# Kernel optimization log

Measured on AMD Instinct MI355X. Metric: run time of the kernel, lower is better.

## Reference

```python
import jax, jax.numpy as jnp
import numpy as np

B, S, H = 2, 1024, 2048
HEADS = 16
QC = 1536      # q_compressed_dim
KVC = 512      # kv_compressed_dim
ROPE = 64      # qk_rope_dim
NOPE = H // HEADS  # 128, non-rope head dim
VH = 128       # v_head_dim
INTER = 1408   # MoE intermediate dim
NSH = 2        # shared experts
NRT = 8        # routed experts
TOPK = 2
EPS = 1e-6


def setup_inputs() -> dict:
    key = jax.random.key(0)
    ks = jax.random.split(key, 16)

    def w(k, shape, scale=0.02):
        return jax.random.normal(k, shape, jnp.float32) * scale

    return {
        "x": jax.random.normal(ks[0], (B, S, H), jnp.float32),
        "freq": jax.random.uniform(ks[1], (S, ROPE // 2), jnp.float32, 0.0, 2.0 * np.pi),
        "mask": jnp.zeros((S, S), jnp.float32),
        "w_attn_norm": jnp.ones((H,), jnp.float32),
        "w_ffn_norm": jnp.ones((H,), jnp.float32),
        "W_dq": w(ks[2], (H, QC)),
        "q_c_norm": jnp.ones((QC,), jnp.float32),
        "W_uq": w(ks[3], (QC, HEADS * (NOPE + ROPE))),
        "W_dkv": w(ks[4], (H, KVC + ROPE)),
        "kv_c_norm": jnp.ones((KVC,), jnp.float32),
        "W_ukv": w(ks[5], (KVC, HEADS * (NOPE + VH))),
        "W_o": w(ks[6], (HEADS * VH, H)),
        "W_r": w(ks[7], (H, NRT)),
        "Ws_gate": w(ks[8], (NSH, H, INTER)),
        "Ws_up": w(ks[9], (NSH, H, INTER)),
        "Ws_down": w(ks[10], (NSH, INTER, H)),
        "We_gate": w(ks[11], (NRT, H, INTER)),
        "We_up": w(ks[12], (NRT, H, INTER)),
        "We_down": w(ks[13], (NRT, INTER, H)),
    }


def rmsnorm(x, w):
    return x * jax.lax.rsqrt(jnp.mean(x * x, axis=-1, keepdims=True) + EPS) * w


def rope_apply(x, cos, sin):
    # x: [..., S, D]; cos/sin: [S, D/2], interleaved-pair rotation
    x1 = x[..., 0::2]
    x2 = x[..., 1::2]
    return jnp.stack([x1 * cos - x2 * sin, x1 * sin + x2 * cos], axis=-1).reshape(x.shape)


def _experts(t, Wg, Wu, Wd):
    # t: [T,H]; W*: [E,H,I]/[E,I,H] -> [E,T,H], SwiGLU per expert
    hid = jax.nn.silu(jnp.einsum('th,ehi->eti', t, Wg)) * jnp.einsum('th,ehi->eti', t, Wu)
    return jnp.einsum('eti,eih->eth', hid, Wd)


def reference(x, freq, mask, w_attn_norm, w_ffn_norm, W_dq, q_c_norm, W_uq, W_dkv,
              kv_c_norm, W_ukv, W_o, W_r, Ws_gate, Ws_up, Ws_down,
              We_gate, We_up, We_down):
    Bb, Ss, Hh = x.shape
    cos = jnp.cos(freq)
    sin = jnp.sin(freq)

    # ---- MLA attention (pre-norm) ----
    h = rmsnorm(x, w_attn_norm)
    cq = rmsnorm(h @ W_dq, q_c_norm)                              # [B,S,QC]
    q = (cq @ W_uq).reshape(Bb, Ss, HEADS, NOPE + ROPE).transpose(0, 2, 1, 3)
    q_nope, q_rope = q[..., :NOPE], q[..., NOPE:]
    q_rope = rope_apply(q_rope, cos, sin)                          # [B,Hh,S,ROPE]

    ckv = h @ W_dkv                                               # [B,S,KVC+ROPE]
    kv_c = rmsnorm(ckv[..., :KVC], kv_c_norm)
    k_rope = rope_apply(ckv[..., KVC:], cos, sin)                  # [B,S,ROPE] shared over heads
    kv = (kv_c @ W_ukv).reshape(Bb, Ss, HEADS, NOPE + VH).transpose(0, 2, 1, 3)
    k_nope, v = kv[..., :NOPE], kv[..., NOPE:]

    scale = 1.0 / np.sqrt(NOPE + ROPE)
    scores = (jnp.einsum('bhsd,bhtd->bhst', q_nope, k_nope)
              + jnp.einsum('bhsd,btd->bhst', q_rope, k_rope)) * scale + mask
    attn = jax.nn.softmax(scores, axis=-1)
    attn_out = jnp.einsum('bhst,bhtd->bshd', attn, v).reshape(Bb, Ss, HEADS * VH) @ W_o
    x = x + attn_out

    # ---- DeepSeekMoE FFN (pre-norm) ----
    t = rmsnorm(x, w_ffn_norm).reshape(Bb * Ss, Hh)
    shared = _experts(t, Ws_gate, Ws_up, Ws_down).sum(axis=0)      # [T,H]
    probs = jax.nn.softmax(t @ W_r, axis=-1)                       # [T,E]
    vals, idx = jax.lax.top_k(probs, TOPK)
    weights = (jax.nn.one_hot(idx, NRT, dtype=t.dtype) * vals[..., None]).sum(axis=1)  # [T,E]
    routed = jnp.einsum('eth,te->th', _experts(t, We_gate, We_up, We_down), weights)
    return x + (shared + routed).reshape(Bb, Ss, Hh)
```

## Files before the change

### kernel.cpp

```cpp
#include <hip/hip_runtime.h>

typedef __bf16 bf16;
typedef _Float16 f16;
typedef unsigned short u16;
typedef __bf16 bf16x8 __attribute__((ext_vector_type(8)));
typedef _Float16 f16x8 __attribute__((ext_vector_type(8)));
typedef unsigned short u16x8 __attribute__((ext_vector_type(8)));
typedef float f32x4 __attribute__((ext_vector_type(4)));

#define TOK   2048
#define SEQ   1024
#define HIDD  2048
#define NHEADS 16
#define QCD   1536
#define KVCD  512
#define ROPED 64
#define NOPED 128
#define QDIM  192
#define VHD   128
#define KVD   576
#define KVDP  640
#define INTERD 1408
#define GUD   2816
#define RMS_EPS 1e-6f
#define SPS   64.0f
#define OSC   (1.0f/4096.0f)

__device__ inline void split64(float v, f16& h, f16& l) {
    v *= SPS; h = (f16)v; l = (f16)(v - (float)h);
}

__device__ inline void gl_lds16(const void* g, void* l) {
    __builtin_amdgcn_global_load_lds(
        (const __attribute__((address_space(1))) void*)g,
        (__attribute__((address_space(3))) void*)l,
        16, 0, 0);
}

#define WAITN(N) asm volatile("s_waitcnt vmcnt(" #N ")" ::: "memory")

__global__ __launch_bounds__(256) void tconv_ex3_kernel(const float* __restrict__ gate,
                                                        const float* __restrict__ up,
                                                        const float* __restrict__ down,
                                                        bf16* __restrict__ dGU,
                                                        bf16* __restrict__ dD) {
    const float* src; bf16* dst; int K, N;
    if (blockIdx.z == 0)      { src = gate; dst = dGU;                          K = HIDD;   N = INTERD; }
    else if (blockIdx.z == 1) { src = up;   dst = dGU + (size_t)INTERD * HIDD;  K = HIDD;   N = INTERD; }
    else                      { src = down; dst = dD;                           K = INTERD; N = HIDD; }
    int nb = blockIdx.x * 32, kb = blockIdx.y * 32;
    if (nb >= N || kb >= K) return;
    __shared__ float tile[32][33];
    int tx = threadIdx.x & 31, ty = threadIdx.x >> 5;
#pragma unroll
    for (int i = 0; i < 32; i += 8)
        tile[ty + i][tx] = src[(long)(kb + ty + i) * N + nb + tx];
    __syncthreads();
#pragma unroll
    for (int i = 0; i < 32; i += 8)
        dst[(long)(nb + ty + i) * K + kb + tx] = (bf16)tile[tx][ty + i];
}

__global__ __launch_bounds__(256) void tconv3h_kernel(const float* __restrict__ src,
                                                      f16* __restrict__ dst,
                                                      int K, int N, int Npad) {
    __shared__ float tile[32][33];
    int nb = blockIdx.x * 32, kb = blockIdx.y * 32;
    int tx = threadIdx.x & 31, ty = threadIdx.x >> 5;
#pragma unroll
    for (int i = 0; i < 32; i += 8) {
        int k = kb + ty + i, n = nb + tx;
        tile[ty + i][tx] = (k < K && n < N) ? src[(long)k * N + n] : 0.f;
    }
    __syncthreads();
#pragma unroll
    for (int i = 0; i < 32; i += 8) {
        int n = nb + ty + i, k = kb + tx;
        if (n < Npad && k < K) {
            f16 h, l; split64(tile[tx][ty + i], h, l);
            long base = (long)n * (3 * K) + k;
            dst[base] = h; dst[base + K] = l; dst[base + 2 * K] = h;
        }
    }
}

template<int F16, int TM, int TN>
__global__ __launch_bounds__(256) void gemm_bt_kernel(
    const u16* __restrict__ A, const u16* __restrict__ B, void* __restrict__ Cv,
    const float* __restrict__ aux, const int* __restrict__ idx,
    const int* __restrict__ cntPtr,
    int K, int lda, int ldb, int ldc,
    long sA, long sB, long sC,
    int mode, int auxLd, float osc)
{
    constexpr int AM = TM / 32;
    constexpr int AN = TN / 32;
    constexpr int NBUF = (TM + TN > 192) ? 2 : 3;
    constexpr int PF = NBUF - 1;
    constexpr int L = TM / 32 + TN / 32;
    __shared__ u16 As[NBUF][TM * 64];
    __shared__ u16 Bs[NBUF][TN * 64];
    const int bn = blockIdx.x, bm = blockIdx.y, z = blockIdx.z;
    int cnt = 1 << 30;
    if (cntPtr) {
        cnt = *cntPtr;
        int pad = (cnt + TM - 1) & ~(TM - 1);
        if (bm * TM >= pad) return;
    }
    const int tid = threadIdx.x, lane = tid & 63, w = tid >> 6;
    const int wm = w >> 1, wn = w & 1;
    const int lr = lane & 15;
    const int srow = lane >> 3, c16 = lane & 7;
    const u16* Ab = A + (long)z * sA + (long)bm * TM * lda;
    const u16* Bb = B + (long)z * sB + (long)bn * TN * ldb;
    f32x4 acc[AM][AN] = {};

    auto stage = [&](int buf, int k0) {
#pragma unroll
        for (int i = 0; i < TM / 32; i++) {
            int rb = i * 32 + w * 8;
            int row = rb + srow;
            int gc = ((c16 ^ (row & 7)) << 3);
            gl_lds16(&Ab[(long)row * lda + k0 + gc], &As[buf][rb * 64]);
        }
#pragma unroll
        for (int i = 0; i < TN / 32; i++) {
            int rb = i * 32 + w * 8;
            int row = rb + srow;
            int gc = ((c16 ^ (row & 7)) << 3);
            gl_lds16(&Bb[(long)row * ldb + k0 + gc], &Bs[buf][rb * 64]);
        }
    };

    const int nk = K >> 6;
#pragma unroll
    for (int p = 0; p < PF; ++p) if (p < nk) stage(p, p << 6);

    for (int t = 0; t < nk; ++t) {
        if (t + PF < nk) stage((t + PF) % NBUF, (t + PF) << 6);
        const int inflight = (nk - 1 - t < PF) ? (nk - 1 - t) : PF;
        if (inflight >= 2) {
            if constexpr (L == 4) WAITN(8); else if constexpr (L == 6) WAITN(12); else WAITN(16);
        } else if (inflight == 1) {
            if constexpr (L == 4) WAITN(4); else if constexpr (L == 6) WAITN(6); else WAITN(8);
        } else {
            WAITN(0);
        }
        __builtin_amdgcn_s_barrier();
        __builtin_amdgcn_sched_barrier(0);
        const int cur = t % NBUF;
#pragma unroll
        for (int ks = 0; ks < 2; ks++) {
            u16x8 af[AM], bfr[AN];
#pragma unroll
            for (int mi = 0; mi < AM; mi++) {
                int row = wm * (TM / 2) + mi * 16 + lr;
                int cg = (ks * 4 + (lane >> 4)) ^ (row & 7);
                af[mi] = *(const u16x8*)&As[cur][row * 64 + cg * 8];
            }
#pragma unroll
            for (int ni = 0; ni < AN; ni++) {
                int row = wn * (TN / 2) + ni * 16 + lr;
                int cg = (ks * 4 + (lane >> 4)) ^ (row & 7);
                bfr[ni] = *(const u16x8*)&Bs[cur][row * 64 + cg * 8];
            }
#pragma unroll
            for (int mi = 0; mi < AM; mi++)
#pragma unroll
                for (int ni = 0; ni < AN; ni++) {
                    if constexpr (F16)
                        acc[mi][ni] = __builtin_amdgcn_mfma_f32_16x16x32_f16(
                            __builtin_bit_cast(f16x8, af[mi]),
                            __builtin_bit_cast(f16x8, bfr[ni]), acc[mi][ni], 0, 0, 0);
                    else
                        acc[mi][ni] = __builtin_amdgcn_mfma_f32_16x16x32_bf16(
                            __builtin_bit_cast(bf16x8, af[mi]),
                            __builtin_bit_cast(bf16x8, bfr[ni]), acc[mi][ni], 0, 0, 0);
                }
        }
        __builtin_amdgcn_s_barrier();
    }

    const int r0 = (lane >> 4) << 2;
    const int rowBase = bm * TM + wm * (TM / 2);
    const int colBase = bn * TN + wn * (TN / 2);
#pragma unroll
    for (int mi = 0; mi < AM; mi++) {
#pragma unroll
        for (int ni = 0; ni < AN; ni++) {
#pragma unroll
            for (int r = 0; r < 4; r++) {
                int row = rowBase + mi * 16 + r0 + r;
                int col = colBase + ni * 16 + lr;
                float val = acc[mi][ni][r] * osc;
                long ci = (long)z * sC + (long)row * ldc + col;
                if (mode == 0) {
                    ((float*)Cv)[ci] = val;
                } else if (mode == 2) {
                    ((float*)Cv)[ci] = val + aux[(long)row * auxLd + col];
                } else if (mode == 3) {
                    float s = aux ? aux[(long)row * auxLd] : 1.f;
                    ((float*)Cv)[ci] += s * val;
                } else if (mode == 5) {
                    if (row < cnt) {
                        int tok = idx[row];
                        ((float*)Cv)[(long)tok * ldc + col] += aux[(long)tok * auxLd] * val;
                    }
                } else {
                    f16 h = (f16)val; f16 l = (f16)(val - (float)h);
                    ((f16*)Cv)[ci] = h; ((f16*)Cv)[ci + auxLd] = h; ((f16*)Cv)[ci + 2 * auxLd] = l;
                }
            }
        }
    }
}

__global__ __launch_bounds__(256) void rmsnorm_kernel(const float* __restrict__ in,
                                                      const float* __restrict__ w,
                                                      bf16* __restrict__ outB,
                                                      float* __restrict__ copyOut, int C) {
    long row = blockIdx.x;
    const float* r = in + row * C;
    float ss = 0.f;
    for (int i = threadIdx.x; i < C; i += 256) { float v = r[i]; ss += v * v; }
    for (int off = 32; off > 0; off >>= 1) ss += __shfl_down(ss, off, 64);
    __shared__ float red[5];
    int lane = threadIdx.x & 63, wv = threadIdx.x >> 6;
    if (lane == 0) red[wv] = ss;
    __syncthreads();
    if (threadIdx.x == 0) red[4] = rsqrtf((red[0] + red[1] + red[2] + red[3]) / C + RMS_EPS);
    __syncthreads();
    float sc = red[4];
    for (int i = threadIdx.x; i < C; i += 256) {
        outB[row * C + i] = (bf16)(r[i] * sc * w[i]);
        if (copyOut) copyOut[row * C + i] = r[i];
    }
}

__global__ __launch_bounds__(256) void rmsnorm3h_kernel(const float* __restrict__ in,
                                                        const float* __restrict__ w,
                                                        f16* __restrict__ out3, int C) {
    long row = blockIdx.x;
    const float* r = in + row * C;
    float ss = 0.f;
    for (int i = threadIdx.x; i < C; i += 256) { float v = r[i]; ss += v * v; }
    for (int off = 32; off > 0; off >>= 1) ss += __shfl_down(ss, off, 64);
    __shared__ float red[5];
    int lane = threadIdx.x & 63, wv = threadIdx.x >> 6;
    if (lane == 0) red[wv] = ss;
    __syncthreads();
    if (threadIdx.x == 0) red[4] = rsqrtf((red[0] + red[1] + red[2] + red[3]) / C + RMS_EPS);
    __syncthreads();
    float sc = red[4];
    f16* o = out3 + row * (3L * C);
    for (int i = threadIdx.x; i < C; i += 256) {
        f16 h, l; split64(r[i] * sc * w[i], h, l);
        o[i] = h; o[C + i] = h; o[2 * C + i] = l;
    }
}

__global__ __launch_bounds__(256) void kvsplit3h_kernel(const float* __restrict__ ckv,
                                                        const float* __restrict__ nrm,
                                                        const float* __restrict__ freq,
                                                        f16* __restrict__ kvc3,
                                                        float* __restrict__ krope) {
    int t = blockIdx.x; int s = t & (SEQ - 1);
    const float* r = ckv + (long)t * KVDP;
    float ss = 0.f;
    for (int i = threadIdx.x; i < KVCD; i += 256) { float v = r[i]; ss += v * v; }
    for (int off = 32; off > 0; off >>= 1) ss += __shfl_down(ss, off, 64);
    __shared__ float red[5];
    int lane = threadIdx.x & 63, wv = threadIdx.x >> 6;
    if (lane == 0) red[wv] = ss;
    __syncthreads();
    if (threadIdx.x == 0) red[4] = rsqrtf((red[0] + red[1] + red[2] + red[3]) / KVCD + RMS_EPS);
    __syncthreads();
    float sc = red[4];
    f16* o = kvc3 + (long)t * (3 * KVCD);
    for (int i = threadIdx.x; i < KVCD; i += 256) {
        f16 h, l; split64(r[i] * sc * nrm[i], h, l);
        o[i] = h; o[KVCD + i] = h; o[2 * KVCD + i] = l;
    }
    if (threadIdx.x < 32) {
        int i = threadIdx.x;
        float f = freq[s * 32 + i], c = cosf(f), sn = sinf(f);
        float x1 = r[KVCD + 2 * i], x2 = r[KVCD + 2 * i + 1];
        krope[(long)t * ROPED + 2 * i]     = x1 * c - x2 * sn;
        krope[(long)t * ROPED + 2 * i + 1] = x1 * sn + x2 * c;
    }
}

__global__ __launch_bounds__(256) void build_q3h_kernel(const float* __restrict__ qpre,
                                                        const float* __restrict__ freq,
                                                        f16* __restrict__ q3) {
    int t = blockIdx.x; int b = t >> 10, s = t & (SEQ - 1);
    for (int idx = threadIdx.x; idx < NHEADS * 96; idx += 256) {
        int h = idx / 96, j = idx % 96;
        const float* qrow = qpre + (long)t * 3072 + h * QDIM;
        f16* dst = q3 + ((long)(b * NHEADS + h) * SEQ + s) * (3 * QDIM);
        if (j < 64) {
            int d = 2 * j;
#pragma unroll
            for (int u = 0; u < 2; u++) {
                f16 hh, ll; split64(qrow[d + u], hh, ll);
                dst[d + u] = hh; dst[QDIM + d + u] = hh; dst[2 * QDIM + d + u] = ll;
            }
        } else {
            int i = j - 64;
            float f = freq[s * 32 + i], c = cosf(f), sn = sinf(f);
            float x1 = qrow[NOPED + 2 * i], x2 = qrow[NOPED + 2 * i + 1];
            float v0 = x1 * c - x2 * sn, v1 = x1 * sn + x2 * c;
            int d = NOPED + 2 * i;
            f16 h0, l0, h1, l1; split64(v0, h0, l0); split64(v1, h1, l1);
            dst[d] = h0; dst[QDIM + d] = h0; dst[2 * QDIM + d] = l0;
            dst[d + 1] = h1; dst[QDIM + d + 1] = h1; dst[2 * QDIM + d + 1] = l1;
        }
    }
}

__global__ __launch_bounds__(256) void build_k3h_kernel(const float* __restrict__ kv,
                                                        const float* __restrict__ krope,
                                                        f16* __restrict__ k3,
                                                        f16* __restrict__ v3T) {
    int t = blockIdx.x; int b = t >> 10, s = t & (SEQ - 1);
    const float* kvrow = kv + (long)t * 4096;
    const float* kr = krope + (long)t * ROPED;
    for (int idx = threadIdx.x; idx < NHEADS * 96; idx += 256) {
        int h = idx / 96, j = idx % 96;
        f16* dst = k3 + ((long)(b * NHEADS + h) * SEQ + s) * (3 * QDIM);
        float v0, v1; int d;
        if (j < 64) { d = 2 * j; v0 = kvrow[h * 256 + d]; v1 = kvrow[h * 256 + d + 1]; }
        else { int i = j - 64; d = NOPED + 2 * i; v0 = kr[2 * i]; v1 = kr[2 * i + 1]; }
        f16 h0, l0, h1, l1; split64(v0, h0, l0); split64(v1, h1, l1);
        dst[d] = h0; dst[QDIM + d] = l0; dst[2 * QDIM + d] = h0;
        dst[d + 1] = h1; dst[QDIM + d + 1] = l1; dst[2 * QDIM + d + 1] = h1;
    }
    for (int idx = threadIdx.x; idx < NHEADS * VHD; idx += 256) {
        int h = idx >> 7, d = idx & 127;
        f16 hh, ll; split64(kvrow[h * 256 + NOPED + d], hh, ll);
        long base = ((long)(b * NHEADS + h) * VHD + d) * (3 * SEQ) + s;
        v3T[base] = hh; v3T[base + SEQ] = ll; v3T[base + 2 * SEQ] = hh;
    }
}

__global__ __launch_bounds__(256) void softmax3h_kernel(const float* __restrict__ scores,
                                                        const float* __restrict__ mask,
                                                        f16* __restrict__ P3, float scale) {
    int s = blockIdx.x, h = blockIdx.y;
    const float* row  = scores + ((long)h * SEQ + s) * SEQ;
    const float* mrow = mask + (long)s * SEQ;
    f16* prow = P3 + ((long)h * SEQ + s) * (3 * SEQ);
    float v[4]; float m = -1e30f;
#pragma unroll
    for (int j = 0; j < 4; j++) {
        int i = threadIdx.x + j * 256;
        v[j] = row[i] * scale + mrow[i];
        m = fmaxf(m, v[j]);
    }
    for (int off = 32; off > 0; off >>= 1) m = fmaxf(m, __shfl_down(m, off, 64));
    __shared__ float redm[5], reds[5];
    int lane = threadIdx.x & 63, wv = threadIdx.x >> 6;
    if (lane == 0) redm[wv] = m;
    __syncthreads();
    if (threadIdx.x == 0) redm[4] = fmaxf(fmaxf(redm[0], redm[1]), fmaxf(redm[2], redm[3]));
    __syncthreads();
    float M = redm[4];
    float sum = 0.f;
#pragma unroll
    for (int j = 0; j < 4; j++) { v[j] = expf(v[j] - M); sum += v[j]; }
    for (int off = 32; off > 0; off >>= 1) sum += __shfl_down(sum, off, 64);
    if (lane == 0) reds[wv] = sum;
    __syncthreads();
    if (threadIdx.x == 0) reds[4] = reds[0] + reds[1] + reds[2] + reds[3];
    __syncthreads();
    float inv = 1.f / reds[4];
#pragma unroll
    for (int j = 0; j < 4; j++) {
        int i = threadIdx.x + j * 256;
        f16 hh, ll; split64(v[j] * inv, hh, ll);
        prow[i] = hh; prow[SEQ + i] = hh; prow[2 * SEQ + i] = ll;
    }
}

__global__ void zero_counts_kernel(int* counts) {
    if (threadIdx.x < 8) counts[threadIdx.x] = 0;
}

__global__ __launch_bounds__(64) void router_kernel(const float* __restrict__ x2,
                                                    const float* __restrict__ wffn,
                                                    const float* __restrict__ Wr,
                                                    float* __restrict__ wts,
                                                    int* __restrict__ perm,
                                                    int* __restrict__ counts) {
    int t = blockIdx.x; int lane = threadIdx.x;
    const float* r = x2 + (long)t * HIDD;
    float ss = 0.f;
    for (int k = lane; k < HIDD; k += 64) { float v = r[k]; ss += v * v; }
    for (int off = 32; off > 0; off >>= 1) ss += __shfl_down(ss, off, 64);
    float sc = rsqrtf(__shfl(ss, 0, 64) / HIDD + RMS_EPS);
    float acc[8] = {0, 0, 0, 0, 0, 0, 0, 0};
    for (int k = lane; k < HIDD; k += 64) {
        float tv = r[k] * sc * wffn[k];
        const float* wr = Wr + (long)k * 8;
#pragma unroll
        for (int e = 0; e < 8; e++) acc[e] += tv * wr[e];
    }
#pragma unroll
    for (int e = 0; e < 8; e++)
        for (int off = 32; off > 0; off >>= 1) acc[e] += __shfl_down(acc[e], off, 64);
    if (lane == 0) {
        float m = acc[0];
#pragma unroll
        for (int e = 1; e < 8; e++) m = fmaxf(m, acc[e]);
        float p[8]; float se = 0.f;
#pragma unroll
        for (int e = 0; e < 8; e++) { p[e] = expf(acc[e] - m); se += p[e]; }
        float inv = 1.f / se;
        int i1 = 0; float v1 = p[0];
        for (int e = 1; e < 8; e++) if (p[e] > v1) { v1 = p[e]; i1 = e; }
        int i2 = -1; float v2 = -1.f;
        for (int e = 0; e < 8; e++) if (e != i1 && p[e] > v2) { v2 = p[e]; i2 = e; }
#pragma unroll
        for (int e = 0; e < 8; e++)
            wts[(long)t * 8 + e] = (e == i1) ? v1 * inv : ((e == i2) ? v2 * inv : 0.f);
        int s1 = atomicAdd(&counts[i1], 1); perm[i1 * TOK + s1] = t;
        int s2 = atomicAdd(&counts[i2], 1); perm[i2 * TOK + s2] = t;
    }
}

__global__ __launch_bounds__(256) void gather_kernel(const bf16* __restrict__ tbuf,
                                                     const int* __restrict__ perm,
                                                     const int* __restrict__ cntPtr,
                                                     bf16* __restrict__ tA) {
    int row = blockIdx.x;
    int cnt = *cntPtr;
    int pad = (cnt + 127) & ~127;
    if (row >= pad) return;
    int i = threadIdx.x * 8;
    if (row < cnt) {
        int tok = perm[row];
        *(bf16x8*)&tA[(long)row * HIDD + i] = *(const bf16x8*)&tbuf[(long)tok * HIDD + i];
    } else {
        bf16x8 z = {};
        *(bf16x8*)&tA[(long)row * HIDD + i] = z;
    }
}

__global__ __launch_bounds__(256) void silumul_kernel(const float* __restrict__ gu,
                                                      bf16* __restrict__ hid,
                                                      const int* __restrict__ cntPtr) {
    long t = blockIdx.x;
    if (cntPtr) {
        int pad = (*cntPtr + 127) & ~127;
        if (t >= pad) return;
    }
    const float* row = gu + t * GUD;
    bf16* h = hid + t * INTERD;
    for (int i = threadIdx.x; i < INTERD; i += 256) {
        float g = row[i], u = row[INTERD + i];
        h[i] = (bf16)(g / (1.f + expf(-g)) * u);
    }
}

static inline size_t alignup(size_t v) { return (v + 255) & ~(size_t)255; }

extern "C" void kernel_launch(void* const* d_in, const int* in_sizes, int n_in,
                              void* d_out, int out_size, void* d_ws, size_t ws_size,
                              hipStream_t stream) {
    const float* x       = (const float*)d_in[0];
    const float* freq    = (const float*)d_in[1];
    const float* mask    = (const float*)d_in[2];
    const float* w_attn  = (const float*)d_in[3];
    const float* w_ffn   = (const float*)d_in[4];
    const float* W_dq    = (const float*)d_in[5];
    const float* q_c_nrm = (const float*)d_in[6];
    const float* W_uq    = (const float*)d_in[7];
    const float* W_dkv   = (const float*)d_in[8];
    const float* kv_nrm  = (const float*)d_in[9];
    const float* W_ukv   = (const float*)d_in[10];
    const float* W_o     = (const float*)d_in[11];
    const float* W_r     = (const float*)d_in[12];
    const float* Ws_gate = (const float*)d_in[13];
    const float* Ws_up   = (const float*)d_in[14];
    const float* Ws_down = (const float*)d_in[15];
    const float* We_gate = (const float*)d_in[16];
    const float* We_up   = (const float*)d_in[17];
    const float* We_down = (const float*)d_in[18];
    float* out = (float*)d_out;
    char* ws = (char*)d_ws;
    (void)in_sizes; (void)n_in; (void)out_size;

    size_t o = 0;
    auto alloc = [&](size_t n) { size_t r = o; o += alignup(n); return r; };
    size_t oWslot = alloc((size_t)3072 * 3 * QCD * 2);
    size_t oQ3    = alloc((size_t)32 * SEQ * 3 * QDIM * 2);
    size_t oK3    = alloc((size_t)32 * SEQ * 3 * QDIM * 2);
    size_t oV3T   = alloc((size_t)32 * VHD * 3 * SEQ * 2);
    size_t oAttn3 = alloc((size_t)TOK * 3 * HIDD * 2);
    size_t oX2    = alloc((size_t)TOK * HIDD * 4);
    size_t oTbuf  = alloc((size_t)TOK * HIDD * 2);
    size_t oTA    = alloc((size_t)TOK * HIDD * 2);
    size_t oWts   = alloc((size_t)TOK * 8 * 4);
    size_t oPerm  = alloc((size_t)8 * TOK * 4);
    size_t oCnt   = alloc((size_t)8 * 4);
    size_t oKrope = alloc((size_t)TOK * ROPED * 4);
    size_t zH3   = alignup((size_t)TOK * 3 * HIDD * 2);
    size_t zCqp  = alignup((size_t)TOK * QCD * 4);
    size_t zCq3  = alignup((size_t)TOK * 3 * QCD * 2);
    size_t zQp   = alignup((size_t)TOK * 3072 * 4);
    size_t zCkv  = alignup((size_t)TOK * KVDP * 4);
    size_t zKvc3 = alignup((size_t)TOK * 3 * KVCD * 2);
    size_t zKv   = alignup((size_t)TOK * 4096 * 4);
    size_t chain = zH3 + zCqp + zCq3 + zQp + zCkv + zKvc3 + zKv;
    size_t zScores = alignup((size_t)16 * SEQ * SEQ * 4);
    size_t zP3     = alignup((size_t)16 * SEQ * 3 * SEQ * 2);
    size_t zGu     = alignup((size_t)TOK * GUD * 4);
    size_t zHid    = alignup((size_t)TOK * INTERD * 2);
    size_t arenaSz = chain;
    if (zScores + zP3 > arenaSz) arenaSz = zScores + zP3;
    if (zGu + zHid > arenaSz) arenaSz = zGu + zHid;
    size_t oArena = alloc(arenaSz);
    if (ws_size < o) return;

    size_t oH3   = oArena;
    size_t oCqp  = oH3 + zH3;
    size_t oCq3  = oCqp + zCqp;
    size_t oQp   = oCq3 + zCq3;
    size_t oCkv  = oQp + zQp;
    size_t oKvc3 = oCkv + zCkv;
    size_t oKv   = oKvc3 + zKvc3;
    size_t oScores = oArena;
    size_t oP3     = oArena + zScores;
    size_t oGu     = oArena;
    size_t oHid    = oArena + zGu;

    f16*  wslotH = (f16*)(ws + oWslot);
    bf16* wslotB = (bf16*)(ws + oWslot);
    bf16* wslotB2 = (bf16*)(ws + oWslot + (size_t)GUD * HIDD * 2);
    f16*  q3    = (f16*)(ws + oQ3);
    f16*  k3    = (f16*)(ws + oK3);
    f16*  v3T   = (f16*)(ws + oV3T);
    f16*  attn3 = (f16*)(ws + oAttn3);
    float* x2   = (float*)(ws + oX2);
    bf16* tbuf  = (bf16*)(ws + oTbuf);
    bf16* tA    = (bf16*)(ws + oTA);
    float* wts  = (float*)(ws + oWts);
    int*  perm  = (int*)(ws + oPerm);
    int*  counts = (int*)(ws + oCnt);
    float* krope = (float*)(ws + oKrope);
    f16*  h3    = (f16*)(ws + oH3);
    float* cqpre = (float*)(ws + oCqp);
    f16*  cq3   = (f16*)(ws + oCq3);
    float* qpre = (float*)(ws + oQp);
    float* ckv  = (float*)(ws + oCkv);
    f16*  kvc3  = (f16*)(ws + oKvc3);
    float* kv   = (float*)(ws + oKv);
    float* scores = (float*)(ws + oScores);
    f16*  P3    = (f16*)(ws + oP3);
    float* gu   = (float*)(ws + oGu);
    bf16* hid   = (bf16*)(ws + oHid);

    auto tconv3h = [&](const float* src, f16* dst, int K, int N, int Npad) {
        dim3 g((Npad + 31) / 32, (K + 31) / 32);
        tconv3h_kernel<<<g, 256, 0, stream>>>(src, dst, K, N, Npad);
    };
    auto tconvEx = [&](const float* gate, const float* up, const float* down) {
        tconv_ex3_kernel<<<dim3(64, 64, 3), 256, 0, stream>>>(gate, up, down, wslotB, wslotB2);
    };
    auto gH128x128 = [&](const f16* A, const f16* B, void* C, const float* aux,
                         int M, int N, int K, int lda, int ldb, int ldc,
                         long sA, long sB, long sC, int Z, int mode, int auxLd, float osc) {
        dim3 g(N / 128, M / 128, Z);
        gemm_bt_kernel<1, 128, 128><<<g, 256, 0, stream>>>((const u16*)A, (const u16*)B, C, aux,
            nullptr, nullptr, K, lda, ldb, ldc, sA, sB, sC, mode, auxLd, osc);
    };
    auto gH128x64 = [&](const f16* A, const f16* B, void* C, const float* aux,
                        int M, int N, int K, int lda, int ldb, int ldc,
                        long sA, long sB, long sC, int Z, int mode, int auxLd, float osc) {
        dim3 g(N / 64, M / 128, Z);
        gemm_bt_kernel<1, 128, 64><<<g, 256, 0, stream>>>((const u16*)A, (const u16*)B, C, aux,
            nullptr, nullptr, K, lda, ldb, ldc, sA, sB, sC, mode, auxLd, osc);
    };
    auto gH64x64 = [&](const f16* A, const f16* B, void* C, const float* aux,
                       int M, int N, int K, int lda, int ldb, int ldc,
                       long sA, long sB, long sC, int Z, int mode, int auxLd, float osc) {
        dim3 g(N / 64, M / 64, Z);
        gemm_bt_kernel<1, 64, 64><<<g, 256, 0, stream>>>((const u16*)A, (const u16*)B, C, aux,
            nullptr, nullptr, K, lda, ldb, ldc, sA, sB, sC, mode, auxLd, osc);
    };
    auto gB128x64 = [&](const bf16* A, const bf16* B, void* C,
                        const float* aux, const int* idx, const int* cnt,
                        int M, int N, int K, int lda, int ldb, int ldc, int mode, int auxLd) {
        dim3 g(N / 64, M / 128, 1);
        gemm_bt_kernel<0, 128, 64><<<g, 256, 0, stream>>>((const u16*)A, (const u16*)B, C, aux,
            idx, cnt, K, lda, ldb, ldc, 0, 0, 0, mode, auxLd, 1.0f);
    };
    auto gB64x64 = [&](const bf16* A, const bf16* B, void* C,
                       const float* aux, const int* idx, const int* cnt,
                       int M, int N, int K, int lda, int ldb, int ldc, int mode, int auxLd) {
        dim3 g(N / 64, M / 64, 1);
        gemm_bt_kernel<0, 64, 64><<<g, 256, 0, stream>>>((const u16*)A, (const u16*)B, C, aux,
            idx, cnt, K, lda, ldb, ldc, 0, 0, 0, mode, auxLd, 1.0f);
    };

    rmsnorm3h_kernel<<<TOK, 256, 0, stream>>>(x, w_attn, h3, HIDD);

    tconv3h(W_dq, wslotH, HIDD, QCD, QCD);
    gH128x64(h3, wslotH, cqpre, nullptr, TOK, QCD, 3 * HIDD, 3 * HIDD, 3 * HIDD, QCD,
             0, 0, 0, 1, 0, 0, OSC);
    rmsnorm3h_kernel<<<TOK, 256, 0, stream>>>(cqpre, q_c_nrm, cq3, QCD);

    tconv3h(W_uq, wslotH, QCD, 3072, 3072);
    gH128x64(cq3, wslotH, qpre, nullptr, TOK, 3072, 3 * QCD, 3 * QCD, 3 * QCD, 3072,
             0, 0, 0, 1, 0, 0, OSC);

    tconv3h(W_dkv, wslotH, HIDD, KVD, KVDP);
    gH64x64(h3, wslotH, ckv, nullptr, TOK, KVDP, 3 * HIDD, 3 * HIDD, 3 * HIDD, KVDP,
            0, 0, 0, 1, 0, 0, OSC);
    kvsplit3h_kernel<<<TOK, 256, 0, stream>>>(ckv, kv_nrm, freq, kvc3, krope);

    tconv3h(W_ukv, wslotH, KVCD, 4096, 4096);
    gH128x128(kvc3, wslotH, kv, nullptr, TOK, 4096, 3 * KVCD, 3 * KVCD, 3 * KVCD, 4096,
              0, 0, 0, 1, 0, 0, OSC);

    build_q3h_kernel<<<TOK, 256, 0, stream>>>(qpre, freq, q3);
    build_k3h_kernel<<<TOK, 256, 0, stream>>>(kv, krope, k3, v3T);

    for (int b = 0; b < 2; b++) {
        int h0 = b * NHEADS;
        gH128x128(q3 + (size_t)h0 * SEQ * 3 * QDIM, k3 + (size_t)h0 * SEQ * 3 * QDIM,
                  scores, nullptr, SEQ, SEQ, 3 * QDIM, 3 * QDIM, 3 * QDIM, SEQ,
                  (long)SEQ * 3 * QDIM, (long)SEQ * 3 * QDIM, (long)SEQ * SEQ, 16, 0, 0, OSC);
        softmax3h_kernel<<<dim3(SEQ, 16), 256, 0, stream>>>(scores, mask, P3,
                                                            1.f / sqrtf((float)QDIM));
        gH64x64(P3, v3T + (size_t)h0 * VHD * 3 * SEQ,
                attn3 + (size_t)b * SEQ * 3 * HIDD, nullptr,
                SEQ, VHD, 3 * SEQ, 3 * SEQ, 3 * SEQ, 3 * HIDD,
                (long)SEQ * 3 * SEQ, (long)VHD * 3 * SEQ, (long)VHD, 16, 6, HIDD,
                1.0f / SPS);
    }

    tconv3h(W_o, wslotH, HIDD, HIDD, HIDD);
    gH128x64(attn3, wslotH, x2, x, TOK, HIDD, 3 * HIDD, 3 * HIDD, 3 * HIDD, HIDD,
             0, 0, 0, 1, 2, HIDD, OSC);

    rmsnorm_kernel<<<TOK, 256, 0, stream>>>(x2, w_ffn, tbuf, out, HIDD);
    zero_counts_kernel<<<1, 64, 0, stream>>>(counts);
    router_kernel<<<TOK, 64, 0, stream>>>(x2, w_ffn, W_r, wts, perm, counts);

    for (int e = 0; e < 2; e++) {
        tconvEx(Ws_gate + (size_t)e * HIDD * INTERD,
                Ws_up   + (size_t)e * HIDD * INTERD,
                Ws_down + (size_t)e * INTERD * HIDD);
        gB128x64(tbuf, wslotB, gu, nullptr, nullptr, nullptr,
                 TOK, GUD, HIDD, HIDD, HIDD, GUD, 0, 0);
        silumul_kernel<<<TOK, 256, 0, stream>>>(gu, hid, nullptr);
        gB128x64(hid, wslotB2, out, nullptr, nullptr, nullptr,
                 TOK, HIDD, INTERD, INTERD, INTERD, HIDD, 3, 0);
    }
    for (int e = 0; e < 8; e++) {
        gather_kernel<<<TOK, 256, 0, stream>>>(tbuf, perm + (size_t)e * TOK, counts + e, tA);
        tconvEx(We_gate + (size_t)e * HIDD * INTERD,
                We_up   + (size_t)e * HIDD * INTERD,
                We_down + (size_t)e * INTERD * HIDD);
        gB64x64(tA, wslotB, gu, nullptr, nullptr, counts + e,
                TOK, GUD, HIDD, HIDD, HIDD, GUD, 0, 0);
        silumul_kernel<<<TOK, 256, 0, stream>>>(gu, hid, counts + e);
        gB64x64(hid, wslotB2, out, wts + e, perm + (size_t)e * TOK, counts + e,
                TOK, HIDD, INTERD, INTERD, INTERD, HIDD, 5, 8);
    }
}
```

Before: 1.645 ms.

## Fuse SiLU-mul into gate/up GEMM epilogue, batch expert gathers, restructure GEMM pipeline

Gate and up weight rows are now interleaved during the transpose, so adjacent GEMM output columns hold a gate/up pair. A new epilogue mode combines each pair with a lane shuffle and writes bf16 SiLU(g)*u directly. This removes the fp32 gu buffer and the separate silumul kernels. The eight per-expert gathers become one batched kernel writing into a larger per-expert staging buffer. The GEMM main loop is also reordered to issue the next prefetch after the barrier and to drop the trailing barrier when PF==2, at some risk to correctness of the LDS buffer reuse.

```diff
diff --git a/kernel.cpp b/kernel.cpp
--- a/kernel.cpp
+++ b/kernel.cpp
@@ -44,10 +44,10 @@
                                                         const float* __restrict__ down,
                                                         bf16* __restrict__ dGU,
                                                         bf16* __restrict__ dD) {
-    const float* src; bf16* dst; int K, N;
-    if (blockIdx.z == 0)      { src = gate; dst = dGU;                          K = HIDD;   N = INTERD; }
-    else if (blockIdx.z == 1) { src = up;   dst = dGU + (size_t)INTERD * HIDD;  K = HIDD;   N = INTERD; }
-    else                      { src = down; dst = dD;                           K = INTERD; N = HIDD; }
+    const float* src; bf16* dst; int K, N, rowMul, rowAdd;
+    if (blockIdx.z == 0)      { src = gate; dst = dGU; K = HIDD;   N = INTERD; rowMul = 2; rowAdd = 0; }
+    else if (blockIdx.z == 1) { src = up;   dst = dGU; K = HIDD;   N = INTERD; rowMul = 2; rowAdd = 1; }
+    else                      { src = down; dst = dD;  K = INTERD; N = HIDD;   rowMul = 1; rowAdd = 0; }
     int nb = blockIdx.x * 32, kb = blockIdx.y * 32;
     if (nb >= N || kb >= K) return;
     __shared__ float tile[32][33];
@@ -57,8 +57,10 @@
         tile[ty + i][tx] = src[(long)(kb + ty + i) * N + nb + tx];
     __syncthreads();
 #pragma unroll
-    for (int i = 0; i < 32; i += 8)
-        dst[(long)(nb + ty + i) * K + kb + tx] = (bf16)tile[tx][ty + i];
+    for (int i = 0; i < 32; i += 8) {
+        int n = nb + ty + i;
+        dst[(long)(n * rowMul + rowAdd) * K + kb + tx] = (bf16)tile[tx][ty + i];
+    }
 }
 
 __global__ __launch_bounds__(256) void tconv3h_kernel(const float* __restrict__ src,
@@ -131,24 +133,7 @@
             gl_lds16(&Bb[(long)row * ldb + k0 + gc], &Bs[buf][rb * 64]);
         }
     };
-
-    const int nk = K >> 6;
-#pragma unroll
-    for (int p = 0; p < PF; ++p) if (p < nk) stage(p, p << 6);
-
-    for (int t = 0; t < nk; ++t) {
-        if (t + PF < nk) stage((t + PF) % NBUF, (t + PF) << 6);
-        const int inflight = (nk - 1 - t < PF) ? (nk - 1 - t) : PF;
-        if (inflight >= 2) {
-            if constexpr (L == 4) WAITN(8); else if constexpr (L == 6) WAITN(12); else WAITN(16);
-        } else if (inflight == 1) {
-            if constexpr (L == 4) WAITN(4); else if constexpr (L == 6) WAITN(6); else WAITN(8);
-        } else {
-            WAITN(0);
-        }
-        __builtin_amdgcn_s_barrier();
-        __builtin_amdgcn_sched_barrier(0);
-        const int cur = t % NBUF;
+    auto compute = [&](int cur) {
 #pragma unroll
         for (int ks = 0; ks < 2; ks++) {
             u16x8 af[AM], bfr[AN];
@@ -178,7 +163,31 @@
                             __builtin_bit_cast(bf16x8, bfr[ni]), acc[mi][ni], 0, 0, 0);
                 }
         }
-        __builtin_amdgcn_s_barrier();
+    };
+
+    const int nk = K >> 6;
+#pragma unroll
+    for (int p = 0; p < PF; ++p) if (p < nk) stage(p, p << 6);
+
+    if constexpr (PF == 2) {
+        for (int t = 0; t < nk; ++t) {
+            if (t < nk - 1) { if constexpr (L == 4) WAITN(4); else WAITN(6); }
+            else            WAITN(0);
+            __builtin_amdgcn_s_barrier();
+            __builtin_amdgcn_sched_barrier(0);
+            if (t + PF < nk) stage((t + PF) % NBUF, (t + PF) << 6);
+            compute(t % NBUF);
+        }
+    } else {
+        for (int t = 0; t < nk; ++t) {
+            if (t + 1 < nk) stage((t + 1) & 1, (t + 1) << 6);
+            if (t + 1 < nk) WAITN(8);
+            else            WAITN(0);
+            __builtin_amdgcn_s_barrier();
+            __builtin_amdgcn_sched_barrier(0);
+            compute(t & 1);
+            __builtin_amdgcn_s_barrier();
+        }
     }
 
     const int r0 = (lane >> 4) << 2;
@@ -206,6 +215,13 @@
                         int tok = idx[row];
                         ((float*)Cv)[(long)tok * ldc + col] += aux[(long)tok * auxLd] * val;
                     }
+                } else if (mode == 7) {
+                    float other = __shfl_xor(val, 1, 64);
+                    if (!(lane & 1)) {
+                        float g = val, u = other;
+                        ((bf16*)Cv)[(long)row * auxLd + (col >> 1)] =
+                            (bf16)(g / (1.f + expf(-g)) * u);
+                    }
                 } else {
                     f16 h = (f16)val; f16 l = (f16)(val - (float)h);
                     ((f16*)Cv)[ci] = h; ((f16*)Cv)[ci + auxLd] = h; ((f16*)Cv)[ci + 2 * auxLd] = l;
@@ -428,37 +444,22 @@
     }
 }
 
-__global__ __launch_bounds__(256) void gather_kernel(const bf16* __restrict__ tbuf,
-                                                     const int* __restrict__ perm,
-                                                     const int* __restrict__ cntPtr,
-                                                     bf16* __restrict__ tA) {
-    int row = blockIdx.x;
-    int cnt = *cntPtr;
+__global__ __launch_bounds__(256) void gather8_kernel(const bf16* __restrict__ tbuf,
+                                                      const int* __restrict__ perm,
+                                                      const int* __restrict__ counts,
+                                                      bf16* __restrict__ tA8) {
+    int e = blockIdx.y, row = blockIdx.x;
+    int cnt = counts[e];
     int pad = (cnt + 127) & ~127;
     if (row >= pad) return;
+    bf16* tA = tA8 + (size_t)e * TOK * HIDD;
     int i = threadIdx.x * 8;
     if (row < cnt) {
-        int tok = perm[row];
+        int tok = perm[e * TOK + row];
         *(bf16x8*)&tA[(long)row * HIDD + i] = *(const bf16x8*)&tbuf[(long)tok * HIDD + i];
     } else {
         bf16x8 z = {};
         *(bf16x8*)&tA[(long)row * HIDD + i] = z;
-    }
-}
-
-__global__ __launch_bounds__(256) void silumul_kernel(const float* __restrict__ gu,
-                                                      bf16* __restrict__ hid,
-                                                      const int* __restrict__ cntPtr) {
-    long t = blockIdx.x;
-    if (cntPtr) {
-        int pad = (*cntPtr + 127) & ~127;
-        if (t >= pad) return;
-    }
-    const float* row = gu + t * GUD;
-    bf16* h = hid + t * INTERD;
-    for (int i = threadIdx.x; i < INTERD; i += 256) {
-        float g = row[i], u = row[INTERD + i];
-        h[i] = (bf16)(g / (1.f + expf(-g)) * u);
     }
 }
 
@@ -499,7 +500,6 @@
     size_t oAttn3 = alloc((size_t)TOK * 3 * HIDD * 2);
     size_t oX2    = alloc((size_t)TOK * HIDD * 4);
     size_t oTbuf  = alloc((size_t)TOK * HIDD * 2);
-    size_t oTA    = alloc((size_t)TOK * HIDD * 2);
     size_t oWts   = alloc((size_t)TOK * 8 * 4);
     size_t oPerm  = alloc((size_t)8 * TOK * 4);
     size_t oCnt   = alloc((size_t)8 * 4);
@@ -514,11 +514,11 @@
     size_t chain = zH3 + zCqp + zCq3 + zQp + zCkv + zKvc3 + zKv;
     size_t zScores = alignup((size_t)16 * SEQ * SEQ * 4);
     size_t zP3     = alignup((size_t)16 * SEQ * 3 * SEQ * 2);
-    size_t zGu     = alignup((size_t)TOK * GUD * 4);
+    size_t zTA8    = alignup((size_t)8 * TOK * HIDD * 2);
     size_t zHid    = alignup((size_t)TOK * INTERD * 2);
     size_t arenaSz = chain;
     if (zScores + zP3 > arenaSz) arenaSz = zScores + zP3;
-    if (zGu + zHid > arenaSz) arenaSz = zGu + zHid;
+    if (zTA8 + zHid > arenaSz) arenaSz = zTA8 + zHid;
     size_t oArena = alloc(arenaSz);
     if (ws_size < o) return;
 
@@ -531,8 +531,8 @@
     size_t oKv   = oKvc3 + zKvc3;
     size_t oScores = oArena;
     size_t oP3     = oArena + zScores;
-    size_t oGu     = oArena;
-    size_t oHid    = oArena + zGu;
+    size_t oTA8    = oArena;
+    size_t oHid    = oArena + zTA8;
 
     f16*  wslotH = (f16*)(ws + oWslot);
     bf16* wslotB = (bf16*)(ws + oWslot);
@@ -543,7 +543,6 @@
     f16*  attn3 = (f16*)(ws + oAttn3);
     float* x2   = (float*)(ws + oX2);
     bf16* tbuf  = (bf16*)(ws + oTbuf);
-    bf16* tA    = (bf16*)(ws + oTA);
     float* wts  = (float*)(ws + oWts);
     int*  perm  = (int*)(ws + oPerm);
     int*  counts = (int*)(ws + oCnt);
@@ -557,7 +556,7 @@
     float* kv   = (float*)(ws + oKv);
     float* scores = (float*)(ws + oScores);
     f16*  P3    = (f16*)(ws + oP3);
-    float* gu   = (float*)(ws + oGu);
+    bf16* tA8   = (bf16*)(ws + oTA8);
     bf16* hid   = (bf16*)(ws + oHid);
 
     auto tconv3h = [&](const float* src, f16* dst, int K, int N, int Npad) {
@@ -647,25 +646,23 @@
     rmsnorm_kernel<<<TOK, 256, 0, stream>>>(x2, w_ffn, tbuf, out, HIDD);
     zero_counts_kernel<<<1, 64, 0, stream>>>(counts);
     router_kernel<<<TOK, 64, 0, stream>>>(x2, w_ffn, W_r, wts, perm, counts);
+    gather8_kernel<<<dim3(TOK, 8), 256, 0, stream>>>(tbuf, perm, counts, tA8);
 
     for (int e = 0; e < 2; e++) {
         tconvEx(Ws_gate + (size_t)e * HIDD * INTERD,
                 Ws_up   + (size_t)e * HIDD * INTERD,
                 Ws_down + (size_t)e * INTERD * HIDD);
-        gB128x64(tbuf, wslotB, gu, nullptr, nullptr, nullptr,
-                 TOK, GUD, HIDD, HIDD, HIDD, GUD, 0, 0);
-        silumul_kernel<<<TOK, 256, 0, stream>>>(gu, hid, nullptr);
+        gB128x64(tbuf, wslotB, hid, nullptr, nullptr, nullptr,
+                 TOK, GUD, HIDD, HIDD, HIDD, GUD, 7, INTERD);
         gB128x64(hid, wslotB2, out, nullptr, nullptr, nullptr,
                  TOK, HIDD, INTERD, INTERD, INTERD, HIDD, 3, 0);
     }
     for (int e = 0; e < 8; e++) {
-        gather_kernel<<<TOK, 256, 0, stream>>>(tbuf, perm + (size_t)e * TOK, counts + e, tA);
         tconvEx(We_gate + (size_t)e * HIDD * INTERD,
                 We_up   + (size_t)e * HIDD * INTERD,
                 We_down + (size_t)e * INTERD * HIDD);
-        gB64x64(tA, wslotB, gu, nullptr, nullptr, counts + e,
-                TOK, GUD, HIDD, HIDD, HIDD, GUD, 0, 0);
-        silumul_kernel<<<TOK, 256, 0, stream>>>(gu, hid, counts + e);
+        gB64x64(tA8 + (size_t)e * TOK * HIDD, wslotB, hid, nullptr, nullptr, counts + e,
+                TOK, GUD, HIDD, HIDD, HIDD, GUD, 7, INTERD);
         gB64x64(hid, wslotB2, out, wts + e, perm + (size_t)e * TOK, counts + e,
                 TOK, HIDD, INTERD, INTERD, INTERD, HIDD, 5, 8);
     }
```

Result: slower. 1.710 ms (+3.9%).
